# Performance work log

Hardware: AMD Instinct MI355X
Metric: run time of the kernel (lower is better)

The kernel has to match this reference:

```python
import jax, jax.numpy as jnp
import numpy as np


def _hilbert_d2xy(n, d):
    # standard Hilbert curve: distance d -> (x, y) on n x n grid (n power of 2)
    x = y = 0
    t = d
    s = 1
    while s < n:
        rx = 1 & (t // 2)
        ry = 1 & (t ^ rx)
        if ry == 0:
            if rx == 1:
                x = s - 1 - x
                y = s - 1 - y
            x, y = y, x
        x += s * rx
        y += s * ry
        t //= 4
        s *= 2
    return x, y


def _hilbert_perm(seq_len):
    n = int(round(np.sqrt(seq_len)))
    assert n * n == seq_len
    perm = np.empty(seq_len, dtype=np.int32)
    for d in range(seq_len):
        x, y = _hilbert_d2xy(n, d)
        perm[d] = y * n + x  # linear (row-major) index visited at Hilbert step d
    return perm


def setup_inputs() -> dict:
    key = jax.random.key(0)
    k1, k2, k3 = jax.random.split(key, 3)
    B, S, H, D = 1, 4096, 8, 64
    q = jax.random.normal(k1, (B, S, H, D), dtype=jnp.float32)
    k = jax.random.normal(k2, (B, S, H, D), dtype=jnp.float32)
    v = jax.random.normal(k3, (B, S, H, D), dtype=jnp.float32)
    hilbert_perm = jnp.asarray(_hilbert_perm(S))
    return {"q": q, "k": k, "v": v, "hilbert_perm": hilbert_perm}


def reference(q, k, v, hilbert_perm):
    B, S, H, D = q.shape
    inv_perm = jnp.argsort(hilbert_perm)

    # apply_hilbert_ordering along dim=1 (seq): gather by permutation
    q_o = q[:, hilbert_perm]
    k_o = k[:, hilbert_perm]
    v_o = v[:, hilbert_perm]

    # faithful to original: raw flat reshape of [B,S,H,D] -> [B*H, S, D]
    q_f = q_o.reshape(B * H, S, D)
    k_f = k_o.reshape(B * H, S, D)
    v_f = v_o.reshape(B * H, S, D)

    scale = 1.0 / jnp.sqrt(jnp.asarray(D, dtype=q.dtype))
    scores = jnp.einsum('bsd,btd->bst', q_f, k_f) * scale  # [B*H, S, S]
    attn = jax.nn.softmax(scores, axis=-1)
    out_f = jnp.einsum('bst,btd->bsd', attn, v_f)  # [B*H, S, D]

    out = out_f.reshape(B, H, S, D).transpose(0, 2, 1, 3).reshape(B, S, H, D)
    # inverse Hilbert ordering along dim=1
    return out[:, inv_perm]
```

## Files before the change

### kernel.cpp

```cpp
#include <hip/hip_runtime.h>

typedef _Float16 f16;
typedef _Float16 f16x4 __attribute__((ext_vector_type(4)));
typedef _Float16 f16x8 __attribute__((ext_vector_type(8)));
typedef __fp16 fp16x2 __attribute__((ext_vector_type(2)));
typedef float f32x4 __attribute__((ext_vector_type(4)));

#define MFMA_16x16x32_F16(A, B, C) __builtin_amdgcn_mfma_f32_16x16x32_f16((A), (B), (C), 0, 0, 0)

typedef const __attribute__((address_space(1))) char gchar;
typedef __attribute__((address_space(3))) char lchar;

__device__ __forceinline__ float fexp2(float x) { return __builtin_amdgcn_exp2f(x); }
__device__ __forceinline__ int swzb(int b) { return b ^ ((b >> 3) & 0x70); }

namespace {
constexpr int SB = 4096;
constexpr size_t BB = (size_t)SB * 64 * 2;
}

__device__ __forceinline__ int kinv(int r) {
    return 32 * (r >> 5) + 8 * ((r >> 2) & 3) + 4 * ((r >> 4) & 1) + (r & 3);
}

__global__ __launch_bounds__(256)
void hilbert_prepass_kernel(const float* __restrict__ kp, const float* __restrict__ vp,
                            const int* __restrict__ perm,
                            char* __restrict__ kw, char* __restrict__ vtw)
{
    const int bid = blockIdx.x;
    const int batch = bid & 7;
    const int tile = bid >> 3;
    const int tid = (int)threadIdx.x;
    const int r = tid >> 2;
    const int c4 = tid & 3;

    __shared__ float Vl[64][68];

    const int t = tile * 64 + r;
    const int srow = perm[batch * 512 + (t >> 3)];
    const size_t boff = (size_t)srow * 512 + (t & 7) * 64 + c4 * 16;

    {
        const float* ks = kp + boff;
        const float4 k0 = *(const float4*)(ks + 0);
        const float4 k1 = *(const float4*)(ks + 4);
        const float4 k2 = *(const float4*)(ks + 8);
        const float4 k3 = *(const float4*)(ks + 12);
        f16x8 h0, h1;
        h0[0] = (f16)k0.x; h0[1] = (f16)k0.y; h0[2] = (f16)k0.z; h0[3] = (f16)k0.w;
        h0[4] = (f16)k1.x; h0[5] = (f16)k1.y; h0[6] = (f16)k1.z; h0[7] = (f16)k1.w;
        h1[0] = (f16)k2.x; h1[1] = (f16)k2.y; h1[2] = (f16)k2.z; h1[3] = (f16)k2.w;
        h1[4] = (f16)k3.x; h1[5] = (f16)k3.y; h1[6] = (f16)k3.z; h1[7] = (f16)k3.w;
        char* kt = kw + (size_t)batch * BB + (size_t)tile * 8192;
        const int o = r * 128 + c4 * 32;
        *(f16x8*)(kt + swzb(o)) = h0;
        *(f16x8*)(kt + swzb(o + 16)) = h1;
    }
    {
        const float* vs = vp + boff;
        *(float4*)&Vl[r][c4 * 16 + 0]  = *(const float4*)(vs + 0);
        *(float4*)&Vl[r][c4 * 16 + 4]  = *(const float4*)(vs + 4);
        *(float4*)&Vl[r][c4 * 16 + 8]  = *(const float4*)(vs + 8);
        *(float4*)&Vl[r][c4 * 16 + 12] = *(const float4*)(vs + 12);
    }
    __syncthreads();
    {
        const int d = tid >> 2;
        const int a = tid & 3;
        char* vt = vtw + (size_t)batch * BB + (size_t)tile * 8192;
        const int b0 = 32 * (a >> 1) + 4 * (a & 1);
#pragma unroll
        for (int gp = 0; gp < 4; ++gp) {
            f16x4 qv;
#pragma unroll
            for (int v = 0; v < 4; ++v) qv[v] = (f16)Vl[16 * a + 4 * gp + v][d];
            *(f16x4*)(vt + swzb(d * 128 + (b0 + 8 * gp) * 2)) = qv;
        }
    }
}

__global__ __launch_bounds__(512, 2)
void hilbert_attn_kernel(const float* __restrict__ qp,
                         const int* __restrict__ perm,
                         const char* __restrict__ kw, const char* __restrict__ vtw,
                         float* __restrict__ op)
{
    __shared__ __align__(16) char SM[131072];

    const int bid = blockIdx.x;
    const int batch = bid & 7;
    const int qbase = (bid >> 3) * 128;
    const int tid = (int)threadIdx.x;
    const int w = tid >> 6;
    const int lane = tid & 63;
    const int l16 = lane & 15;
    const int g = lane >> 4;
    const int half = w >> 2;
    const int wq = w & 3;
    const int swz = (l16 & 7) << 4;

    f16x8 Qf0[2], Qf1[2];
    {
        constexpr float qscl = 0.125f * 1.44269504088896340736f;
#pragma unroll
        for (int s = 0; s < 2; ++s) {
            const int t = qbase + wq * 32 + s * 16 + l16;
            const int srow = perm[batch * 512 + (t >> 3)];
            const float* src = qp + (size_t)srow * 512 + (t & 7) * 64 + g * 8;
#pragma unroll
            for (int kt = 0; kt < 2; ++kt) {
                const float4 x0 = *(const float4*)(src + 32 * kt);
                const float4 x1 = *(const float4*)(src + 32 * kt + 4);
                f16x8 f;
                f[0] = (f16)(x0.x * qscl); f[1] = (f16)(x0.y * qscl);
                f[2] = (f16)(x0.z * qscl); f[3] = (f16)(x0.w * qscl);
                f[4] = (f16)(x1.x * qscl); f[5] = (f16)(x1.y * qscl);
                f[6] = (f16)(x1.z * qscl); f[7] = (f16)(x1.w * qscl);
                if (s == 0) Qf0[kt] = f; else Qf1[kt] = f;
            }
        }
    }

    f32x4 oacc0[4], oacc1[4];
#pragma unroll
    for (int i = 0; i < 4; ++i) {
        oacc0[i] = (f32x4){0.f, 0.f, 0.f, 0.f};
        oacc1[i] = (f32x4){0.f, 0.f, 0.f, 0.f};
    }
    float lr0 = 0.f, lr1 = 0.f;

    const char* ksrc = kw + (size_t)batch * BB + (size_t)tid * 16;
    const char* vsrc = vtw + (size_t)batch * BB + (size_t)tid * 16;

    {
        lchar* dst = (lchar*)&SM[w << 10];
#pragma unroll
        for (int s2 = 0; s2 < 4; ++s2) {
            __builtin_amdgcn_global_load_lds((gchar*)(ksrc + s2 * 8192), dst + s2 * 8192, 16, 0, 0);
            __builtin_amdgcn_global_load_lds((gchar*)(vsrc + s2 * 8192), dst + 32768 + s2 * 8192, 16, 0, 0);
        }
    }
    __syncthreads();

    for (int it = 0; it < 16; ++it) {
        const int cur = it & 1;

        if (it < 15) {
            const size_t go = (size_t)(it + 1) * 32768;
            lchar* dst = (lchar*)&SM[(cur ^ 1) * 65536 + (w << 10)];
#pragma unroll
            for (int s2 = 0; s2 < 4; ++s2) {
                __builtin_amdgcn_global_load_lds((gchar*)(ksrc + go + s2 * 8192), dst + s2 * 8192, 16, 0, 0);
                __builtin_amdgcn_global_load_lds((gchar*)(vsrc + go + s2 * 8192), dst + 32768 + s2 * 8192, 16, 0, 0);
            }
        }

#pragma unroll
        for (int sub = 0; sub < 2; ++sub) {
            const int tile = 2 * half + sub;
            const int kbb = cur * 65536 + tile * 8192;
            const int vbb = cur * 65536 + 32768 + tile * 8192;

            f32x4 sa0[4], sa1[4];
#pragma unroll
            for (int i = 0; i < 4; ++i) {
                sa0[i] = (f32x4){0.f, 0.f, 0.f, 0.f};
                sa1[i] = (f32x4){0.f, 0.f, 0.f, 0.f};
            }
            __builtin_amdgcn_s_setprio(1);
#pragma unroll
            for (int kt = 0; kt < 2; ++kt) {
#pragma unroll
                for (int mt = 0; mt < 4; ++mt) {
                    const int off = kbb + (l16 + 16 * mt) * 128 + (((g + 4 * kt) * 16) ^ swz);
                    const f16x8 kf = *(const f16x8*)&SM[off];
                    sa0[mt] = MFMA_16x16x32_F16(kf, Qf0[kt], sa0[mt]);
                    sa1[mt] = MFMA_16x16x32_F16(kf, Qf1[kt], sa1[mt]);
                }
            }
            __builtin_amdgcn_s_setprio(0);

            float e0[16], e1[16];
#pragma unroll
            for (int mt = 0; mt < 4; ++mt) {
#pragma unroll
                for (int v = 0; v < 4; ++v) {
                    e0[4 * mt + v] = fexp2(sa0[mt][v]);
                    e1[4 * mt + v] = fexp2(sa1[mt][v]);
                }
            }
#pragma unroll
            for (int i = 0; i < 16; ++i) { lr0 += e0[i]; lr1 += e1[i]; }

            union U8 { f16x8 v; fp16x2 h[4]; };
            U8 p0k0, p0k1, p1k0, p1k1;
#pragma unroll
            for (int i = 0; i < 4; ++i) {
                p0k0.h[i] = __builtin_amdgcn_cvt_pkrtz(e0[2 * i], e0[2 * i + 1]);
                p0k1.h[i] = __builtin_amdgcn_cvt_pkrtz(e0[8 + 2 * i], e0[9 + 2 * i]);
                p1k0.h[i] = __builtin_amdgcn_cvt_pkrtz(e1[2 * i], e1[2 * i + 1]);
                p1k1.h[i] = __builtin_amdgcn_cvt_pkrtz(e1[8 + 2 * i], e1[9 + 2 * i]);
            }

            __builtin_amdgcn_s_setprio(1);
#pragma unroll
            for (int kt = 0; kt < 2; ++kt) {
                const f16x8 pf0 = kt ? p0k1.v : p0k0.v;
                const f16x8 pf1 = kt ? p1k1.v : p1k0.v;
#pragma unroll
                for (int mtd = 0; mtd < 4; ++mtd) {
                    const int voff = vbb + (l16 + 16 * mtd) * 128 + (((g + 4 * kt) * 16) ^ swz);
                    const f16x8 vf = *(const f16x8*)&SM[voff];
                    oacc0[mtd] = MFMA_16x16x32_F16(vf, pf0, oacc0[mtd]);
                    oacc1[mtd] = MFMA_16x16x32_F16(vf, pf1, oacc1[mtd]);
                }
            }
            __builtin_amdgcn_s_setprio(0);
        }

        __syncthreads();
    }

    lr0 += __shfl_xor(lr0, 16);
    lr0 += __shfl_xor(lr0, 32);
    lr1 += __shfl_xor(lr1, 16);
    lr1 += __shfl_xor(lr1, 32);

    float* OB = (float*)SM;
    float* ML = (float*)&SM[32768];
    if (w >= 4) {
        float* ob = OB + wq * 2048;
#pragma unroll
        for (int mtd = 0; mtd < 4; ++mtd) {
            *(f32x4*)&ob[l16 * 64 + mtd * 16 + g * 4] = oacc0[mtd];
            *(f32x4*)&ob[(16 + l16) * 64 + mtd * 16 + g * 4] = oacc1[mtd];
        }
        if (g == 0) {
            ML[wq * 32 + l16] = lr0;
            ML[wq * 32 + 16 + l16] = lr1;
        }
    }
    __syncthreads();
    if (w < 4) {
        float* ob = OB + wq * 2048;
#pragma unroll
        for (int s = 0; s < 2; ++s) {
            const float lmine = (s == 0) ? lr0 : lr1;
            const float linv = 1.f / (lmine + ML[wq * 32 + s * 16 + l16]);
            const int t = qbase + wq * 32 + s * 16 + l16;
            const int srow = perm[t];
            float* dst = op + (size_t)srow * 512 + batch * 64 + 4 * g;
#pragma unroll
            for (int mtd = 0; mtd < 4; ++mtd) {
                const f32x4 mine = (s == 0) ? oacc0[mtd] : oacc1[mtd];
                const f32x4 o2 = *(const f32x4*)&ob[(s * 16 + l16) * 64 + mtd * 16 + g * 4];
                float4 o;
                o.x = (mine[0] + o2[0]) * linv;
                o.y = (mine[1] + o2[1]) * linv;
                o.z = (mine[2] + o2[2]) * linv;
                o.w = (mine[3] + o2[3]) * linv;
                *(float4*)(dst + 16 * mtd) = o;
            }
        }
    }
}

extern "C" void kernel_launch(void* const* d_in, const int* in_sizes, int n_in,
                              void* d_out, int out_size, void* d_ws, size_t ws_size,
                              hipStream_t stream) {
    (void)in_sizes; (void)n_in; (void)out_size; (void)ws_size;
    const float* q = (const float*)d_in[0];
    const float* k = (const float*)d_in[1];
    const float* v = (const float*)d_in[2];
    const int* perm = (const int*)d_in[3];
    float* out = (float*)d_out;
    char* kw = (char*)d_ws;
    char* vtw = kw + 8 * BB;
    hipLaunchKernelGGL(hilbert_prepass_kernel, dim3(512), dim3(256), 0, stream,
                       k, v, perm, kw, vtw);
    hipLaunchKernelGGL(hilbert_attn_kernel, dim3(256), dim3(512), 0, stream,
                       q, perm, kw, vtw, out);
}
```

Baseline: 50.93 us.

## Double attention block to 16 waves, one KV subtile per wave

```diff
diff --git a/kernel.cpp b/kernel.cpp
--- a/kernel.cpp
+++ b/kernel.cpp
@@ -80,7 +80,7 @@
     }
 }
 
-__global__ __launch_bounds__(512, 2)
+__global__ __launch_bounds__(1024, 4)
 void hilbert_attn_kernel(const float* __restrict__ qp,
                          const int* __restrict__ perm,
                          const char* __restrict__ kw, const char* __restrict__ vtw,
@@ -96,7 +96,7 @@
     const int lane = tid & 63;
     const int l16 = lane & 15;
     const int g = lane >> 4;
-    const int half = w >> 2;
+    const int q = w >> 2;
     const int wq = w & 3;
     const int swz = (l16 & 7) << 4;
 
@@ -136,88 +136,84 @@
     {
         lchar* dst = (lchar*)&SM[w << 10];
 #pragma unroll
-        for (int s2 = 0; s2 < 4; ++s2) {
-            __builtin_amdgcn_global_load_lds((gchar*)(ksrc + s2 * 8192), dst + s2 * 8192, 16, 0, 0);
-            __builtin_amdgcn_global_load_lds((gchar*)(vsrc + s2 * 8192), dst + 32768 + s2 * 8192, 16, 0, 0);
+        for (int c = 0; c < 2; ++c) {
+            __builtin_amdgcn_global_load_lds((gchar*)(ksrc + c * 16384), dst + c * 16384, 16, 0, 0);
+            __builtin_amdgcn_global_load_lds((gchar*)(vsrc + c * 16384), dst + 32768 + c * 16384, 16, 0, 0);
         }
     }
     __syncthreads();
 
+#pragma unroll 2
     for (int it = 0; it < 16; ++it) {
         const int cur = it & 1;
+        const int kbb = cur * 65536 + q * 8192;
+        const int vbb = cur * 65536 + 32768 + q * 8192;
 
         if (it < 15) {
             const size_t go = (size_t)(it + 1) * 32768;
             lchar* dst = (lchar*)&SM[(cur ^ 1) * 65536 + (w << 10)];
 #pragma unroll
-            for (int s2 = 0; s2 < 4; ++s2) {
-                __builtin_amdgcn_global_load_lds((gchar*)(ksrc + go + s2 * 8192), dst + s2 * 8192, 16, 0, 0);
-                __builtin_amdgcn_global_load_lds((gchar*)(vsrc + go + s2 * 8192), dst + 32768 + s2 * 8192, 16, 0, 0);
-            }
-        }
-
-#pragma unroll
-        for (int sub = 0; sub < 2; ++sub) {
-            const int tile = 2 * half + sub;
-            const int kbb = cur * 65536 + tile * 8192;
-            const int vbb = cur * 65536 + 32768 + tile * 8192;
-
-            f32x4 sa0[4], sa1[4];
-#pragma unroll
-            for (int i = 0; i < 4; ++i) {
-                sa0[i] = (f32x4){0.f, 0.f, 0.f, 0.f};
-                sa1[i] = (f32x4){0.f, 0.f, 0.f, 0.f};
-            }
-            __builtin_amdgcn_s_setprio(1);
-#pragma unroll
-            for (int kt = 0; kt < 2; ++kt) {
-#pragma unroll
-                for (int mt = 0; mt < 4; ++mt) {
-                    const int off = kbb + (l16 + 16 * mt) * 128 + (((g + 4 * kt) * 16) ^ swz);
-                    const f16x8 kf = *(const f16x8*)&SM[off];
-                    sa0[mt] = MFMA_16x16x32_F16(kf, Qf0[kt], sa0[mt]);
-                    sa1[mt] = MFMA_16x16x32_F16(kf, Qf1[kt], sa1[mt]);
-                }
-            }
-            __builtin_amdgcn_s_setprio(0);
-
-            float e0[16], e1[16];
+            for (int c = 0; c < 2; ++c) {
+                __builtin_amdgcn_global_load_lds((gchar*)(ksrc + go + c * 16384), dst + c * 16384, 16, 0, 0);
+                __builtin_amdgcn_global_load_lds((gchar*)(vsrc + go + c * 16384), dst + 32768 + c * 16384, 16, 0, 0);
+            }
+        }
+
+        f32x4 sa0[4], sa1[4];
+#pragma unroll
+        for (int i = 0; i < 4; ++i) {
+            sa0[i] = (f32x4){0.f, 0.f, 0.f, 0.f};
+            sa1[i] = (f32x4){0.f, 0.f, 0.f, 0.f};
+        }
+        __builtin_amdgcn_s_setprio(1);
+#pragma unroll
+        for (int kt = 0; kt < 2; ++kt) {
 #pragma unroll
             for (int mt = 0; mt < 4; ++mt) {
-#pragma unroll
-                for (int v = 0; v < 4; ++v) {
-                    e0[4 * mt + v] = fexp2(sa0[mt][v]);
-                    e1[4 * mt + v] = fexp2(sa1[mt][v]);
-                }
-            }
-#pragma unroll
-            for (int i = 0; i < 16; ++i) { lr0 += e0[i]; lr1 += e1[i]; }
-
-            union U8 { f16x8 v; fp16x2 h[4]; };
-            U8 p0k0, p0k1, p1k0, p1k1;
-#pragma unroll
-            for (int i = 0; i < 4; ++i) {
-                p0k0.h[i] = __builtin_amdgcn_cvt_pkrtz(e0[2 * i], e0[2 * i + 1]);
-                p0k1.h[i] = __builtin_amdgcn_cvt_pkrtz(e0[8 + 2 * i], e0[9 + 2 * i]);
-                p1k0.h[i] = __builtin_amdgcn_cvt_pkrtz(e1[2 * i], e1[2 * i + 1]);
-                p1k1.h[i] = __builtin_amdgcn_cvt_pkrtz(e1[8 + 2 * i], e1[9 + 2 * i]);
-            }
-
-            __builtin_amdgcn_s_setprio(1);
-#pragma unroll
-            for (int kt = 0; kt < 2; ++kt) {
-                const f16x8 pf0 = kt ? p0k1.v : p0k0.v;
-                const f16x8 pf1 = kt ? p1k1.v : p1k0.v;
-#pragma unroll
-                for (int mtd = 0; mtd < 4; ++mtd) {
-                    const int voff = vbb + (l16 + 16 * mtd) * 128 + (((g + 4 * kt) * 16) ^ swz);
-                    const f16x8 vf = *(const f16x8*)&SM[voff];
-                    oacc0[mtd] = MFMA_16x16x32_F16(vf, pf0, oacc0[mtd]);
-                    oacc1[mtd] = MFMA_16x16x32_F16(vf, pf1, oacc1[mtd]);
-                }
-            }
-            __builtin_amdgcn_s_setprio(0);
-        }
+                const int off = kbb + (l16 + 16 * mt) * 128 + (((g + 4 * kt) * 16) ^ swz);
+                const f16x8 kf = *(const f16x8*)&SM[off];
+                sa0[mt] = MFMA_16x16x32_F16(kf, Qf0[kt], sa0[mt]);
+                sa1[mt] = MFMA_16x16x32_F16(kf, Qf1[kt], sa1[mt]);
+            }
+        }
+        __builtin_amdgcn_s_setprio(0);
+
+        float e0[16], e1[16];
+#pragma unroll
+        for (int mt = 0; mt < 4; ++mt) {
+#pragma unroll
+            for (int v = 0; v < 4; ++v) {
+                e0[4 * mt + v] = fexp2(sa0[mt][v]);
+                e1[4 * mt + v] = fexp2(sa1[mt][v]);
+            }
+        }
+#pragma unroll
+        for (int i = 0; i < 16; ++i) { lr0 += e0[i]; lr1 += e1[i]; }
+
+        union U8 { f16x8 v; fp16x2 h[4]; };
+        U8 p0k0, p0k1, p1k0, p1k1;
+#pragma unroll
+        for (int i = 0; i < 4; ++i) {
+            p0k0.h[i] = __builtin_amdgcn_cvt_pkrtz(e0[2 * i], e0[2 * i + 1]);
+            p0k1.h[i] = __builtin_amdgcn_cvt_pkrtz(e0[8 + 2 * i], e0[9 + 2 * i]);
+            p1k0.h[i] = __builtin_amdgcn_cvt_pkrtz(e1[2 * i], e1[2 * i + 1]);
+            p1k1.h[i] = __builtin_amdgcn_cvt_pkrtz(e1[8 + 2 * i], e1[9 + 2 * i]);
+        }
+
+        __builtin_amdgcn_s_setprio(1);
+#pragma unroll
+        for (int kt = 0; kt < 2; ++kt) {
+            const f16x8 pf0 = kt ? p0k1.v : p0k0.v;
+            const f16x8 pf1 = kt ? p1k1.v : p1k0.v;
+#pragma unroll
+            for (int mtd = 0; mtd < 4; ++mtd) {
+                const int voff = vbb + (l16 + 16 * mtd) * 128 + (((g + 4 * kt) * 16) ^ swz);
+                const f16x8 vf = *(const f16x8*)&SM[voff];
+                oacc0[mtd] = MFMA_16x16x32_F16(vf, pf0, oacc0[mtd]);
+                oacc1[mtd] = MFMA_16x16x32_F16(vf, pf1, oacc1[mtd]);
+            }
+        }
+        __builtin_amdgcn_s_setprio(0);
 
         __syncthreads();
     }
@@ -228,38 +224,42 @@
     lr1 += __shfl_xor(lr1, 32);
 
     float* OB = (float*)SM;
-    float* ML = (float*)&SM[32768];
-    if (w >= 4) {
-        float* ob = OB + wq * 2048;
+    float* ML = (float*)&SM[98304];
+    if (q >= 1) {
+        float* ob = OB + ((q - 1) * 4 + wq) * 2048;
 #pragma unroll
         for (int mtd = 0; mtd < 4; ++mtd) {
             *(f32x4*)&ob[l16 * 64 + mtd * 16 + g * 4] = oacc0[mtd];
             *(f32x4*)&ob[(16 + l16) * 64 + mtd * 16 + g * 4] = oacc1[mtd];
         }
         if (g == 0) {
-            ML[wq * 32 + l16] = lr0;
-            ML[wq * 32 + 16 + l16] = lr1;
+            ML[((q - 1) * 4 + wq) * 32 + l16] = lr0;
+            ML[((q - 1) * 4 + wq) * 32 + 16 + l16] = lr1;
         }
     }
     __syncthreads();
-    if (w < 4) {
-        float* ob = OB + wq * 2048;
+    if (q == 0) {
 #pragma unroll
         for (int s = 0; s < 2; ++s) {
-            const float lmine = (s == 0) ? lr0 : lr1;
-            const float linv = 1.f / (lmine + ML[wq * 32 + s * 16 + l16]);
+            float lsum = (s == 0) ? lr0 : lr1;
+#pragma unroll
+            for (int p = 0; p < 3; ++p) lsum += ML[(p * 4 + wq) * 32 + s * 16 + l16];
+            const float linv = 1.f / lsum;
             const int t = qbase + wq * 32 + s * 16 + l16;
             const int srow = perm[t];
             float* dst = op + (size_t)srow * 512 + batch * 64 + 4 * g;
 #pragma unroll
             for (int mtd = 0; mtd < 4; ++mtd) {
-                const f32x4 mine = (s == 0) ? oacc0[mtd] : oacc1[mtd];
-                const f32x4 o2 = *(const f32x4*)&ob[(s * 16 + l16) * 64 + mtd * 16 + g * 4];
+                f32x4 acc = (s == 0) ? oacc0[mtd] : oacc1[mtd];
+#pragma unroll
+                for (int p = 0; p < 3; ++p) {
+                    const f32x4 o2 = *(const f32x4*)&OB[(p * 4 + wq) * 2048 +
+                                                        (s * 16 + l16) * 64 + mtd * 16 + g * 4];
+                    acc[0] += o2[0]; acc[1] += o2[1]; acc[2] += o2[2]; acc[3] += o2[3];
+                }
                 float4 o;
-                o.x = (mine[0] + o2[0]) * linv;
-                o.y = (mine[1] + o2[1]) * linv;
-                o.z = (mine[2] + o2[2]) * linv;
-                o.w = (mine[3] + o2[3]) * linv;
+                o.x = acc[0] * linv; o.y = acc[1] * linv;
+                o.z = acc[2] * linv; o.w = acc[3] * linv;
                 *(float4*)(dst + 16 * mtd) = o;
             }
         }
@@ -279,6 +279,6 @@
     char* vtw = kw + 8 * BB;
     hipLaunchKernelGGL(hilbert_prepass_kernel, dim3(512), dim3(256), 0, stream,
                        k, v, perm, kw, vtw);
-    hipLaunchKernelGGL(hilbert_attn_kernel, dim3(256), dim3(512), 0, stream,
+    hipLaunchKernelGGL(hilbert_attn_kernel, dim3(256), dim3(1024), 0, stream,
                        q, perm, kw, vtw, out);
 }
```

Result: slower. 52.63 us (+3.3%).
